# Performance work log

Measured on AMD Instinct MI355X. Metric: run time of the kernel, lower is better.

The kernel has to match this reference:

```python
import jax, jax.numpy as jnp
import numpy as np

N = 8192        # batch_size == num nodes == num hyperedges
D = 512         # hidden_dim
H_HEADS = 8
HD = D // H_HEADS
TOP_K = 16
EPS = 1e-5      # LayerNorm eps


def setup_inputs() -> dict:
    key = jax.random.key(0)
    ks = jax.random.split(key, 10)
    def rn(k, shape, scale=0.02):
        return jax.random.normal(k, shape, dtype=jnp.float32) * scale
    return {
        "x0": jax.random.normal(ks[0], (N, D), dtype=jnp.float32),
        "x1": jax.random.normal(ks[1], (N, D), dtype=jnp.float32),
        # modality projections: Linear -> ReLU -> LayerNorm (per modality)
        "w_p0": rn(ks[2], (D, D)), "b_p0": jnp.zeros((D,), jnp.float32),
        "g0": jnp.ones((D,), jnp.float32), "beta0": jnp.zeros((D,), jnp.float32),
        "w_p1": rn(ks[3], (D, D)), "b_p1": jnp.zeros((D,), jnp.float32),
        "g1": jnp.ones((D,), jnp.float32), "beta1": jnp.zeros((D,), jnp.float32),
        # MultiheadAttention packed in-proj + out-proj
        "in_w": rn(ks[4], (3 * D, D)), "in_b": jnp.zeros((3 * D,), jnp.float32),
        "out_w": rn(ks[5], (D, D)), "out_b": jnp.zeros((D,), jnp.float32),
        # edge weight predictor MLP
        "ew_w1": rn(ks[6], (D // 2, D)), "ew_b1": jnp.zeros((D // 2,), jnp.float32),
        "ew_w2": rn(ks[7], (1, D // 2)), "ew_b2": jnp.zeros((1,), jnp.float32),
    }


def _layernorm(x, g, b):
    m = x.mean(-1, keepdims=True)
    v = ((x - m) ** 2).mean(-1, keepdims=True)
    return (x - m) * jax.lax.rsqrt(v + EPS) * g + b


def _forward(x0, x1, w_p0, b_p0, g0, beta0, w_p1, b_p1, g1, beta1,
             in_w, in_b, out_w, out_b, ew_w1, ew_b1, ew_w2, ew_b2):
    # per-modality projection: Linear -> ReLU -> LayerNorm
    p0 = _layernorm(jax.nn.relu(x0 @ w_p0.T + b_p0), g0, beta0)
    p1 = _layernorm(jax.nn.relu(x1 @ w_p1.T + b_p1), g1, beta1)
    seq = jnp.stack([p0, p1], axis=1)                       # [N, 2, D]
    # cross-modal MHA (self-attention over the 2 modality tokens)
    qkv = seq @ in_w.T + in_b                               # [N, 2, 3D]
    q, k, v = jnp.split(qkv, 3, axis=-1)
    q = q.reshape(N, 2, H_HEADS, HD)
    k = k.reshape(N, 2, H_HEADS, HD)
    v = v.reshape(N, 2, H_HEADS, HD)
    scores = jnp.einsum('bqhd,bkhd->bhqk', q, k) / jnp.sqrt(jnp.float32(HD))
    attn = jax.nn.softmax(scores, axis=-1)                  # [N, h, 2, 2]
    ctx = jnp.einsum('bhqk,bkhd->bqhd', attn, v).reshape(N, 2, D)
    attended = ctx @ out_w.T + out_b                        # [N, 2, D]
    fused = attended.mean(axis=1)                           # [N, D]
    # node-node attention similarity, row-softmax
    sim = jax.nn.softmax(fused @ fused.T, axis=1)           # [N, N]
    _, idx = jax.lax.top_k(sim, TOP_K)                      # [N, K]
    vals = jnp.take_along_axis(sim, idx, axis=1)            # [N, K]
    rows = jnp.arange(N)
    # H[i,i]=1 first, then H[neighbor, i] = sim[i, neighbor] (may overwrite diag)
    H = jnp.zeros((N, N), sim.dtype).at[rows, rows].set(1.0)
    H = H.at[idx, rows[:, None]].set(vals)
    colsum = H.sum(axis=0)
    H = H.at[rows, rows].set(jnp.where(colsum == 0, 1.0, H[rows, rows]))
    # edge weights
    hidden = jax.nn.relu(fused @ ew_w1.T + ew_b1)
    ew = jax.nn.sigmoid(hidden @ ew_w2.T + ew_b2)[:, 0]     # [N]
    ew = jnp.maximum(ew, 1e-8)
    return H, ew


def reference(x0, x1, w_p0, b_p0, g0, beta0, w_p1, b_p1, g1, beta1,
              in_w, in_b, out_w, out_b, ew_w1, ew_b1, ew_w2, ew_b2):
    return _forward(x0, x1, w_p0, b_p0, g0, beta0, w_p1, b_p1, g1, beta1,
                    in_w, in_b, out_w, out_b, ew_w1, ew_b1, ew_w2, ew_b2)
```

## Files before the change

kernel.cpp:

```cpp
#include <hip/hip_runtime.h>
#include <hip/hip_bf16.h>

#define NN 8192
#define DD 512

typedef unsigned short u16;
typedef __bf16 bf16_t;
typedef bf16_t bf16x8 __attribute__((ext_vector_type(8)));
typedef float f32x4 __attribute__((ext_vector_type(4)));

__device__ __forceinline__ float bf2f(u16 h) {
    union { unsigned u; float f; } v; v.u = ((unsigned)h) << 16; return v.f;
}
__device__ __forceinline__ float bflo(unsigned u) {
    union { unsigned u; float f; } v; v.u = u << 16; return v.f;
}
__device__ __forceinline__ float bfhi(unsigned u) {
    union { unsigned u; float f; } v; v.u = u & 0xFFFF0000u; return v.f;
}
__device__ __forceinline__ u16 f2bf(float f) {
    union { float f; unsigned u; } v; v.f = f;
    unsigned r = v.u + 0x7fffu + ((v.u >> 16) & 1u);
    return (u16)(r >> 16);
}

__global__ __launch_bounds__(256) void cvt7(
        const float* __restrict__ s0, u16* __restrict__ d0,
        const float* __restrict__ s1, u16* __restrict__ d1,
        const float* __restrict__ s2, u16* __restrict__ d2,
        const float* __restrict__ s3, u16* __restrict__ d3,
        const float* __restrict__ s4, u16* __restrict__ d4,
        const float* __restrict__ s5, u16* __restrict__ d5,
        const float* __restrict__ s6, u16* __restrict__ d6) {
    size_t v = ((size_t)blockIdx.x * 256 + threadIdx.x) * 8;
    const float* s; u16* d; size_t off;
    if (v < 4194304)      { s = s0; d = d0; off = v; }
    else if (v < 8388608) { s = s1; d = d1; off = v - 4194304; }
    else if (v < 8650752) { s = s2; d = d2; off = v - 8388608; }
    else if (v < 8912896) { s = s3; d = d3; off = v - 8650752; }
    else if (v < 9699328) { s = s4; d = d4; off = v - 8912896; }
    else if (v < 9961472) { s = s5; d = d5; off = v - 9699328; }
    else                  { s = s6; d = d6; off = v - 9961472; }
    float4 a = *(const float4*)(s + off);
    float4 b = *(const float4*)(s + off + 4);
    ushort4 o0 = make_ushort4(f2bf(a.x), f2bf(a.y), f2bf(a.z), f2bf(a.w));
    ushort4 o1 = make_ushort4(f2bf(b.x), f2bf(b.y), f2bf(b.z), f2bf(b.w));
    *(ushort4*)(d + off) = o0;
    *(ushort4*)(d + off + 4) = o1;
}

#define EPS_LDS 136
template<bool RELU, bool BIAS, bool SPLIT>
__global__ __launch_bounds__(256) void gemm_bt(const u16* __restrict__ A,
        const u16* __restrict__ B, const float* __restrict__ bias,
        const u16* __restrict__ B2, const float* __restrict__ bias2, int halfY,
        u16* __restrict__ C, int M, int Nc, int K) {
    __shared__ alignas(16) u16 Smem[128 * 64 * 2];
    u16* As = Smem;
    u16* Bs = Smem + 128 * 64;
    const int t = threadIdx.x;
    const int lane = t & 63;
    const int wave = t >> 6;
    const int wm = (wave >> 1) * 64;
    const int wn = (wave & 1) * 64;
    const int rowA = blockIdx.y * 128;
    const int rowB = blockIdx.x * 128;
    if (SPLIT && (int)blockIdx.y >= halfY) { B = B2; bias = bias2; }

    f32x4 acc[4][4] = {};
    const int mrow = lane & 15;
    const int kk = (lane >> 4) * 8;

    for (int k0 = 0; k0 < K; k0 += 64) {
        __syncthreads();
        #pragma unroll
        for (int r = 0; r < 4; ++r) {
            int chunk = r * 256 + t;
            const u16* srcA = A + (size_t)(rowA + (chunk >> 3)) * K + k0 + (chunk & 7) * 8;
            __builtin_amdgcn_global_load_lds(
                (const __attribute__((address_space(1))) void*)srcA,
                (__attribute__((address_space(3))) void*)(As + chunk * 8), 16, 0, 0);
            const u16* srcB = B + (size_t)(rowB + (chunk >> 3)) * K + k0 + (chunk & 7) * 8;
            __builtin_amdgcn_global_load_lds(
                (const __attribute__((address_space(1))) void*)srcB,
                (__attribute__((address_space(3))) void*)(Bs + chunk * 8), 16, 0, 0);
        }
        __syncthreads();
        #pragma unroll
        for (int ks = 0; ks < 64; ks += 32) {
            bf16x8 af[4], bfv[4];
            #pragma unroll
            for (int i = 0; i < 4; ++i)
                af[i] = *(const bf16x8*)(As + (wm + i * 16 + mrow) * 64 + ks + kk);
            #pragma unroll
            for (int j = 0; j < 4; ++j)
                bfv[j] = *(const bf16x8*)(Bs + (wn + j * 16 + mrow) * 64 + ks + kk);
            #pragma unroll
            for (int i = 0; i < 4; ++i)
                #pragma unroll
                for (int j = 0; j < 4; ++j)
                    acc[i][j] = __builtin_amdgcn_mfma_f32_16x16x32_bf16(af[i], bfv[j], acc[i][j], 0, 0, 0);
        }
    }

    __syncthreads();
    const int lr0 = (lane >> 4) * 4;
    const int ec0 = wn + (lane & 15);
    #pragma unroll
    for (int h = 0; h < 2; ++h) {
        if ((wave >> 1) == h) {
            #pragma unroll
            for (int j = 0; j < 4; ++j) {
                int c = ec0 + j * 16;
                float bv = BIAS ? bias[rowB + c] : 0.0f;
                #pragma unroll
                for (int i = 0; i < 4; ++i) {
                    #pragma unroll
                    for (int r = 0; r < 4; ++r) {
                        float v = acc[i][j][r] + bv;
                        if (RELU) v = fmaxf(v, 0.0f);
                        Smem[(lr0 + i * 16 + r) * EPS_LDS + c] = f2bf(v);
                    }
                }
            }
        }
        __syncthreads();
        #pragma unroll
        for (int pass = 0; pass < 4; ++pass) {
            int chunk = pass * 256 + t;
            int rloc = chunk >> 4, coff = (chunk & 15) * 8;
            bf16x8 v = *(const bf16x8*)(Smem + rloc * EPS_LDS + coff);
            *(bf16x8*)(C + (size_t)(rowA + h * 64 + rloc) * Nc + rowB + coff) = v;
        }
        __syncthreads();
    }
}

__global__ __launch_bounds__(256) void gemm_qkv(const u16* __restrict__ A,
        const u16* __restrict__ B, const float* __restrict__ bias,
        u16* __restrict__ V, float* __restrict__ scores) {
    __shared__ alignas(16) u16 Smem[128 * 64 * 2];
    u16* As = Smem;
    u16* Bs = Smem + 128 * 64;
    const int t = threadIdx.x;
    const int lane = t & 63;
    const int wave = t >> 6;
    const int wm = (wave >> 1) * 64;
    const int wn = (wave & 1) * 64;
    const int c = blockIdx.x;
    const int rowA = blockIdx.y * 128;
    const bool isQK = (c < 8);

    f32x4 acc[4][4] = {};
    const int mrow = lane & 15;
    const int kk = (lane >> 4) * 8;

    for (int k0 = 0; k0 < DD; k0 += 64) {
        __syncthreads();
        #pragma unroll
        for (int r = 0; r < 4; ++r) {
            int chunk = r * 256 + t;
            int rr = chunk >> 3;
            int brow = isQK ? (c * 64 + rr + ((rr >= 64) ? 448 : 0))
                            : (1024 + (c - 8) * 128 + rr);
            const u16* srcA = A + (size_t)(rowA + rr) * DD + k0 + (chunk & 7) * 8;
            __builtin_amdgcn_global_load_lds(
                (const __attribute__((address_space(1))) void*)srcA,
                (__attribute__((address_space(3))) void*)(As + chunk * 8), 16, 0, 0);
            const u16* srcB = B + (size_t)brow * DD + k0 + (chunk & 7) * 8;
            __builtin_amdgcn_global_load_lds(
                (const __attribute__((address_space(1))) void*)srcB,
                (__attribute__((address_space(3))) void*)(Bs + chunk * 8), 16, 0, 0);
        }
        __syncthreads();
        #pragma unroll
        for (int ks = 0; ks < 64; ks += 32) {
            bf16x8 af[4], bfv[4];
            #pragma unroll
            for (int i = 0; i < 4; ++i)
                af[i] = *(const bf16x8*)(As + (wm + i * 16 + mrow) * 64 + ks + kk);
            #pragma unroll
            for (int j = 0; j < 4; ++j)
                bfv[j] = *(const bf16x8*)(Bs + (wn + j * 16 + mrow) * 64 + ks + kk);
            #pragma unroll
            for (int i = 0; i < 4; ++i)
                #pragma unroll
                for (int j = 0; j < 4; ++j)
                    acc[i][j] = __builtin_amdgcn_mfma_f32_16x16x32_bf16(af[i], bfv[j], acc[i][j], 0, 0, 0);
        }
    }

    __syncthreads();
    const int lr0 = (lane >> 4) * 4;
    const int ec0 = wn + (lane & 15);
    #pragma unroll
    for (int h = 0; h < 2; ++h) {
        if ((wave >> 1) == h) {
            #pragma unroll
            for (int j = 0; j < 4; ++j) {
                int cc = ec0 + j * 16;
                int bcol = isQK ? ((cc < 64) ? c * 64 + cc : 448 + c * 64 + cc)
                                : (1024 + (c - 8) * 128 + cc);
                float bv = bias[bcol];
                #pragma unroll
                for (int i = 0; i < 4; ++i) {
                    #pragma unroll
                    for (int r = 0; r < 4; ++r)
                        Smem[(lr0 + i * 16 + r) * EPS_LDS + cc] = f2bf(acc[i][j][r] + bv);
                }
            }
        }
        __syncthreads();
        if (isQK) {
            if (t < 128) {
                int nd = t >> 2, cb = t & 3, tt2 = cb >> 1, ss = cb & 1;
                const u16* qrow = Smem + (2 * nd + tt2) * EPS_LDS;
                const u16* krow = Smem + (2 * nd + ss) * EPS_LDS + 64;
                float s = 0.0f;
                #pragma unroll
                for (int d8 = 0; d8 < 8; ++d8) {
                    bf16x8 qv = *(const bf16x8*)(qrow + d8 * 8);
                    bf16x8 kv = *(const bf16x8*)(krow + d8 * 8);
                    #pragma unroll
                    for (int u = 0; u < 8; ++u) s += (float)qv[u] * (float)kv[u];
                }
                scores[(size_t)(rowA / 2 + h * 32 + nd) * 32 + c * 4 + cb] = s * 0.125f;
            }
        } else {
            #pragma unroll
            for (int pass = 0; pass < 4; ++pass) {
                int chunk = pass * 256 + t;
                int rloc = chunk >> 4, coff = (chunk & 15) * 8;
                bf16x8 v = *(const bf16x8*)(Smem + rloc * EPS_LDS + coff);
                *(bf16x8*)(V + (size_t)(rowA + h * 64 + rloc) * 512 + (c - 8) * 128 + coff) = v;
            }
        }
        __syncthreads();
    }
}

#define SYM_LDS 129
__global__ __launch_bounds__(256) void gemm_sym(const u16* __restrict__ F,
        u16* __restrict__ C) {
    __shared__ alignas(16) u16 Smem[128 * SYM_LDS];
    const int bx = blockIdx.x, by = blockIdx.y;
    if (bx < by) return;
    u16* As = Smem;
    u16* Bs = Smem + 128 * 64;
    const int t = threadIdx.x;
    const int lane = t & 63;
    const int wave = t >> 6;
    const int wm = (wave >> 1) * 64;
    const int wn = (wave & 1) * 64;
    const int rowI = by * 128;
    const int rowJ = bx * 128;

    f32x4 acc[4][4] = {};
    const int mrow = lane & 15;
    const int kk = (lane >> 4) * 8;

    for (int k0 = 0; k0 < DD; k0 += 64) {
        __syncthreads();
        #pragma unroll
        for (int r = 0; r < 4; ++r) {
            int chunk = r * 256 + t;
            const u16* srcA = F + (size_t)(rowI + (chunk >> 3)) * DD + k0 + (chunk & 7) * 8;
            __builtin_amdgcn_global_load_lds(
                (const __attribute__((address_space(1))) void*)srcA,
                (__attribute__((address_space(3))) void*)(As + chunk * 8), 16, 0, 0);
            const u16* srcB = F + (size_t)(rowJ + (chunk >> 3)) * DD + k0 + (chunk & 7) * 8;
            __builtin_amdgcn_global_load_lds(
                (const __attribute__((address_space(1))) void*)srcB,
                (__attribute__((address_space(3))) void*)(Bs + chunk * 8), 16, 0, 0);
        }
        __syncthreads();
        #pragma unroll
        for (int ks = 0; ks < 64; ks += 32) {
            bf16x8 af[4], bfv[4];
            #pragma unroll
            for (int i = 0; i < 4; ++i)
                af[i] = *(const bf16x8*)(As + (wm + i * 16 + mrow) * 64 + ks + kk);
            #pragma unroll
            for (int j = 0; j < 4; ++j)
                bfv[j] = *(const bf16x8*)(Bs + (wn + j * 16 + mrow) * 64 + ks + kk);
            #pragma unroll
            for (int i = 0; i < 4; ++i)
                #pragma unroll
                for (int j = 0; j < 4; ++j)
                    acc[i][j] = __builtin_amdgcn_mfma_f32_16x16x32_bf16(af[i], bfv[j], acc[i][j], 0, 0, 0);
        }
    }

    __syncthreads();
    const int er0 = wm + (lane >> 4) * 4;
    const int ec0 = wn + (lane & 15);
    #pragma unroll
    for (int j = 0; j < 4; ++j) {
        int c = ec0 + j * 16;
        #pragma unroll
        for (int i = 0; i < 4; ++i) {
            #pragma unroll
            for (int r = 0; r < 4; ++r)
                Smem[(er0 + i * 16 + r) * SYM_LDS + c] = f2bf(acc[i][j][r]);
        }
    }
    __syncthreads();
    #pragma unroll
    for (int pass = 0; pass < 8; ++pass) {
        int chunk = pass * 256 + t;
        int rloc = chunk >> 4, coff = (chunk & 15) * 8;
        union { u16 us[8]; bf16x8 v; } buf;
        #pragma unroll
        for (int k = 0; k < 8; ++k) buf.us[k] = Smem[rloc * SYM_LDS + coff + k];
        *(bf16x8*)(C + (size_t)(rowI + rloc) * NN + rowJ + coff) = buf.v;
    }
    if (bx != by) {
        #pragma unroll
        for (int pass = 0; pass < 8; ++pass) {
            int chunk = pass * 256 + t;
            int tr = chunk >> 4, roff = (chunk & 15) * 8;
            union { u16 us[8]; bf16x8 v; } buf;
            #pragma unroll
            for (int k = 0; k < 8; ++k) buf.us[k] = Smem[(roff + k) * SYM_LDS + tr];
            *(bf16x8*)(C + (size_t)(rowJ + tr) * NN + rowI + roff) = buf.v;
        }
    }
}

__global__ __launch_bounds__(256) void ln2_kernel(const u16* __restrict__ y,
        const float* __restrict__ g0, const float* __restrict__ b0,
        const float* __restrict__ g1, const float* __restrict__ b1,
        u16* __restrict__ seq) {
    int n = blockIdx.x * 4 + (threadIdx.x >> 6);
    int lane = threadIdx.x & 63;
    int modality = n >> 13, node = n & (NN - 1);
    const float* g = modality ? g1 : g0;
    const float* b = modality ? b1 : b0;
    bf16x8 v = *(const bf16x8*)(y + (size_t)n * DD + lane * 8);
    float x[8];
    float s = 0.0f;
    #pragma unroll
    for (int u = 0; u < 8; ++u) { x[u] = (float)v[u]; s += x[u]; }
    #pragma unroll
    for (int off = 32; off; off >>= 1) s += __shfl_xor(s, off);
    float mean = s * (1.0f / DD);
    float vs = 0.0f;
    #pragma unroll
    for (int u = 0; u < 8; ++u) { x[u] -= mean; vs += x[u] * x[u]; }
    #pragma unroll
    for (int off = 32; off; off >>= 1) vs += __shfl_xor(vs, off);
    float inv = rsqrtf(vs * (1.0f / DD) + 1e-5f);
    float4 ga = *(const float4*)(g + lane * 8);
    float4 gb = *(const float4*)(g + lane * 8 + 4);
    float4 ba = *(const float4*)(b + lane * 8);
    float4 bb = *(const float4*)(b + lane * 8 + 4);
    union { u16 us[8]; bf16x8 v; } o;
    o.us[0] = f2bf(x[0] * inv * ga.x + ba.x);
    o.us[1] = f2bf(x[1] * inv * ga.y + ba.y);
    o.us[2] = f2bf(x[2] * inv * ga.z + ba.z);
    o.us[3] = f2bf(x[3] * inv * ga.w + ba.w);
    o.us[4] = f2bf(x[4] * inv * gb.x + bb.x);
    o.us[5] = f2bf(x[5] * inv * gb.y + bb.y);
    o.us[6] = f2bf(x[6] * inv * gb.z + bb.z);
    o.us[7] = f2bf(x[7] * inv * gb.w + bb.w);
    *(bf16x8*)(seq + (size_t)node * (2 * DD) + modality * DD + lane * 8) = o.v;
}

__global__ __launch_bounds__(256) void attn_v(const float* __restrict__ scores,
        const u16* __restrict__ V, u16* __restrict__ ctxm) {
    int n = blockIdx.x * 4 + (threadIdx.x >> 6);
    int lane = threadIdx.x & 63;
    int h = lane >> 3;
    float4 sc = *(const float4*)(scores + (size_t)n * 32 + h * 4);
    float s00 = sc.x, s01 = sc.y, s10 = sc.z, s11 = sc.w;
    float m0 = fmaxf(s00, s01), e00 = __expf(s00 - m0), e01 = __expf(s01 - m0);
    float a00 = e00 / (e00 + e01), a01 = e01 / (e00 + e01);
    float m1 = fmaxf(s10, s11), e10 = __expf(s10 - m1), e11 = __expf(s11 - m1);
    float a10 = e10 / (e10 + e11), a11 = e11 / (e10 + e11);
    float al0 = 0.5f * (a00 + a10), al1 = 0.5f * (a01 + a11);
    bf16x8 v0 = *(const bf16x8*)(V + (size_t)(2 * n) * 512 + lane * 8);
    bf16x8 v1 = *(const bf16x8*)(V + (size_t)(2 * n + 1) * 512 + lane * 8);
    union { u16 us[8]; bf16x8 v; } o;
    #pragma unroll
    for (int u = 0; u < 8; ++u)
        o.us[u] = f2bf(al0 * (float)v0[u] + al1 * (float)v1[u]);
    *(bf16x8*)(ctxm + (size_t)n * 512 + lane * 8) = o.v;
}

__global__ __launch_bounds__(256) void topk_bf16(const u16* __restrict__ S,
        float* __restrict__ topv, int* __restrict__ topi) {
    const float NEG = -3e38f;
    int row = blockIdx.x * 4 + (threadIdx.x >> 6);
    int lane = threadIdx.x & 63;
    const u16* Sr = S + (size_t)row * NN;

    float m = NEG, l = 0.0f;
    float t1v = NEG, t2v = NEG;
    int t1i = 0x7FFFFFFF, t2i = 0x7FFFFFFF;

    #pragma unroll
    for (int p = 0; p < 16; ++p) {
        uint4 raw = *(const uint4*)(Sr + p * 512 + lane * 8);
        int base = p * 512 + lane * 8;
        #pragma unroll
        for (int q = 0; q < 4; ++q) {
            unsigned w = (&raw.x)[q];
            #pragma unroll
            for (int h = 0; h < 2; ++h) {
                float x = h ? bfhi(w) : bflo(w);
                int xi = base + q * 2 + h;
                if (x > m) { l = l * __expf(m - x) + 1.0f; m = x; }
                else l += __expf(x - m);
                bool g1 = x > t1v, g2 = x > t2v;
                t2v = g1 ? t1v : (g2 ? x : t2v);
                t2i = g1 ? t1i : (g2 ? xi : t2i);
                t1v = g1 ? x : t1v;
                t1i = g1 ? xi : t1i;
            }
        }
    }
    #pragma unroll
    for (int off = 32; off; off >>= 1) {
        float om = __shfl_xor(m, off);
        float ol = __shfl_xor(l, off);
        float nm = fmaxf(m, om);
        l = l * __expf(m - nm) + ol * __expf(om - nm);
        m = nm;
    }

    unsigned mk0 = 0, mk1 = 0, mk2 = 0, mk3 = 0;
    float cv = t1v; int ci = t1i;
    float bv = t2v; int bi = t2i;
    for (int r = 0; r < 16; ++r) {
        float wv = cv; int wi = ci;
        #pragma unroll
        for (int off = 32; off; off >>= 1) {
            float ov = __shfl_xor(wv, off);
            int oi = __shfl_xor(wi, off);
            if (ov > wv || (ov == wv && oi < wi)) { wv = ov; wi = oi; }
        }
        if (lane == 0) {
            topv[(size_t)row * 16 + r] = __expf(wv - m) / l;
            topi[(size_t)row * 16 + r] = wi;
        }
        if (wi == ci) {
            int slot = ((wi >> 9) << 3) | (wi & 7);
            unsigned bit = 1u << (slot & 31);
            if (slot < 32) mk0 |= bit; else if (slot < 64) mk1 |= bit;
            else if (slot < 96) mk2 |= bit; else mk3 |= bit;
            cv = bv; ci = bi;
            bv = NEG; bi = 0x7FFFFFFF;
            if (ci == 0x7FFFFFFF) {
                float nb = NEG; int ni = 0x7FFFFFFF;
                #pragma unroll
                for (int p = 0; p < 16; ++p) {
                    uint4 raw = *(const uint4*)(Sr + p * 512 + lane * 8);
                    int base = p * 512 + lane * 8;
                    #pragma unroll
                    for (int q = 0; q < 4; ++q) {
                        unsigned w = (&raw.x)[q];
                        #pragma unroll
                        for (int h = 0; h < 2; ++h) {
                            int sl = p * 8 + q * 2 + h;
                            unsigned mw = (sl < 32) ? mk0 : (sl < 64) ? mk1
                                        : (sl < 96) ? mk2 : mk3;
                            float x = ((mw >> (sl & 31)) & 1u) ? NEG
                                    : (h ? bfhi(w) : bflo(w));
                            if (x > nb) { nb = x; ni = base + q * 2 + h; }
                        }
                    }
                }
                cv = nb; ci = ni;
            }
        }
    }
}

__global__ __launch_bounds__(256) void scatter_diag(const float* __restrict__ topv,
        const int* __restrict__ topi, float* __restrict__ H) {
    int tk = blockIdx.x * 256 + threadIdx.x;
    if (tk < NN * 16) {
        int i = tk >> 4;
        int idx = topi[tk];
        H[(size_t)idx * NN + i] = topv[tk];
    } else {
        int c = tk - NN * 16;
        const int* ti = topi + c * 16;
        bool self = false;
        #pragma unroll
        for (int j = 0; j < 16; ++j) self |= (ti[j] == c);
        if (!self) H[(size_t)c * NN + c] = 1.0f;
    }
}

__global__ __launch_bounds__(256) void ew_kernel(const u16* __restrict__ hidden,
        const float* __restrict__ w2, const float* __restrict__ b2, float* __restrict__ out) {
    int n = blockIdx.x * 4 + (threadIdx.x >> 6);
    int lane = threadIdx.x & 63;
    const u16* hr = hidden + (size_t)n * 256;
    float s = 0.0f;
    #pragma unroll
    for (int p = 0; p < 4; ++p) s += bf2f(hr[lane + p * 64]) * w2[lane + p * 64];
    for (int off = 32; off; off >>= 1) s += __shfl_xor(s, off);
    if (lane == 0) {
        float z = s + b2[0];
        float sig = 1.0f / (1.0f + __expf(-z));
        out[n] = fmaxf(sig, 1e-8f);
    }
}

extern "C" void kernel_launch(void* const* d_in, const int* in_sizes, int n_in,
                              void* d_out, int out_size, void* d_ws, size_t ws_size,
                              hipStream_t stream) {
    const float* x0    = (const float*)d_in[0];
    const float* x1    = (const float*)d_in[1];
    const float* w_p0  = (const float*)d_in[2];
    const float* b_p0  = (const float*)d_in[3];
    const float* g0    = (const float*)d_in[4];
    const float* beta0 = (const float*)d_in[5];
    const float* w_p1  = (const float*)d_in[6];
    const float* b_p1  = (const float*)d_in[7];
    const float* g1    = (const float*)d_in[8];
    const float* beta1 = (const float*)d_in[9];
    const float* in_w  = (const float*)d_in[10];
    const float* in_b  = (const float*)d_in[11];
    const float* out_w = (const float*)d_in[12];
    const float* out_b = (const float*)d_in[13];
    const float* ew_w1 = (const float*)d_in[14];
    const float* ew_b1 = (const float*)d_in[15];
    const float* ew_w2 = (const float*)d_in[16];
    const float* ew_b2 = (const float*)d_in[17];

    float* Hf = (float*)d_out;
    float* ew_out = Hf + (size_t)NN * NN;

    u16* Hu = (u16*)d_out;
    u16* x0b    = Hu;
    u16* x1b    = Hu + 4194304;
    u16* y01    = Hu + 8388608;
    u16* seq    = Hu + 16777216;
    u16* Vbuf   = Hu + 25165824;
    u16* ctxm   = Hu + 50331648;
    u16* hidden = Hu + 54525952;
    float* scB  = (float*)(Hu + 58720256);
    u16* wp0b   = Hu + 60817408;
    u16* wp1b   = wp0b + 262144;
    u16* inwb   = wp1b + 262144;
    u16* outwb  = inwb + 786432;
    u16* eww1b  = outwb + 262144;
    u16* Sb     = Hu + 67108864;
    char* ws = (char*)d_ws;
    u16* fusedB = (u16*)ws;
    float* topv = (float*)(ws + (8u << 20));
    int*   topi = (int*)(ws + (8u << 20) + 524288);

    dim3 blk(256);
    const int BIG = 1 << 30;
    cvt7<<<dim3(4928), blk, 0, stream>>>(x0, x0b, x1, x1b, w_p0, wp0b, w_p1, wp1b,
                                         in_w, inwb, out_w, outwb, ew_w1, eww1b);
    gemm_bt<true, true, true><<<dim3(4, 128), blk, 0, stream>>>(
        x0b, wp0b, b_p0, wp1b, b_p1, 64, y01, 2 * NN, DD, DD);
    ln2_kernel<<<dim3(2 * NN / 4), blk, 0, stream>>>(y01, g0, beta0, g1, beta1, seq);
    gemm_qkv<<<dim3(12, 128), blk, 0, stream>>>(seq, inwb, in_b, Vbuf, scB);
    attn_v<<<dim3(NN / 4), blk, 0, stream>>>(scB, Vbuf, ctxm);
    gemm_bt<false, true, false><<<dim3(4, 64), blk, 0, stream>>>(
        ctxm, outwb, out_b, nullptr, nullptr, BIG, fusedB, NN, DD, DD);
    gemm_bt<true, true, false><<<dim3(2, 64), blk, 0, stream>>>(
        fusedB, eww1b, ew_b1, nullptr, nullptr, BIG, hidden, NN, 256, DD);
    ew_kernel<<<dim3(NN / 4), blk, 0, stream>>>(hidden, ew_w2, ew_b2, ew_out);
    gemm_sym<<<dim3(64, 64), blk, 0, stream>>>(fusedB, Sb);
    topk_bf16<<<dim3(NN / 4), blk, 0, stream>>>(Sb, topv, topi);
    hipMemsetAsync(Hf, 0, (size_t)NN * NN * sizeof(float), stream);
    scatter_diag<<<dim3((NN * 16 + NN) / 256), blk, 0, stream>>>(topv, topi, Hf);
}
```

Measured before the change: 692.6 us.

## Double-buffer gemm_bt K loop and fold edge-weight hidden GEMM into symmetric GEMM

gemm_bt now double-buffers its LDS tiles, so the global-to-LDS load of the next K slice is issued before the MFMA work on the current slice, and its epilogue writes the whole 128x128 tile in one pass instead of two halves. The edge-weight hidden GEMM (fused @ ew_w1^T with bias and ReLU) is folded into the symmetric similarity kernel as extra grid columns, which saves one launch and lets these small blocks run alongside the large sim GEMM. The cost is twice the LDS per block in gemm_bt, which may reduce occupancy, and a branchier combined kernel.

```diff
diff --git a/kernel.cpp b/kernel.cpp
--- a/kernel.cpp
+++ b/kernel.cpp
@@ -55,9 +55,7 @@
         const u16* __restrict__ B, const float* __restrict__ bias,
         const u16* __restrict__ B2, const float* __restrict__ bias2, int halfY,
         u16* __restrict__ C, int M, int Nc, int K) {
-    __shared__ alignas(16) u16 Smem[128 * 64 * 2];
-    u16* As = Smem;
-    u16* Bs = Smem + 128 * 64;
+    __shared__ alignas(16) u16 Smem[2][16384];
     const int t = threadIdx.x;
     const int lane = t & 63;
     const int wave = t >> 6;
@@ -70,9 +68,11 @@
     f32x4 acc[4][4] = {};
     const int mrow = lane & 15;
     const int kk = (lane >> 4) * 8;
-
-    for (int k0 = 0; k0 < K; k0 += 64) {
-        __syncthreads();
+    const int nt = K >> 6;
+
+    auto STAGE = [&](int buf, int k0) {
+        u16* As = Smem[buf];
+        u16* Bs = Smem[buf] + 8192;
         #pragma unroll
         for (int r = 0; r < 4; ++r) {
             int chunk = r * 256 + t;
@@ -85,7 +85,15 @@
                 (const __attribute__((address_space(1))) void*)srcB,
                 (__attribute__((address_space(3))) void*)(Bs + chunk * 8), 16, 0, 0);
         }
-        __syncthreads();
+    };
+
+    STAGE(0, 0);
+    __syncthreads();
+    int cur = 0;
+    for (int ti = 0; ti < nt; ++ti) {
+        if (ti + 1 < nt) STAGE(cur ^ 1, (ti + 1) << 6);
+        const u16* As = Smem[cur];
+        const u16* Bs = Smem[cur] + 8192;
         #pragma unroll
         for (int ks = 0; ks < 64; ks += 32) {
             bf16x8 af[4], bfv[4];
@@ -101,38 +109,34 @@
                 for (int j = 0; j < 4; ++j)
                     acc[i][j] = __builtin_amdgcn_mfma_f32_16x16x32_bf16(af[i], bfv[j], acc[i][j], 0, 0, 0);
         }
-    }
-
+        __syncthreads();
+        cur ^= 1;
+    }
+
+    u16* Ep = &Smem[0][0];
+    const int er0 = wm + (lane >> 4) * 4;
+    const int ec0 = wn + (lane & 15);
+    #pragma unroll
+    for (int j = 0; j < 4; ++j) {
+        int c = ec0 + j * 16;
+        float bv = BIAS ? bias[rowB + c] : 0.0f;
+        #pragma unroll
+        for (int i = 0; i < 4; ++i) {
+            #pragma unroll
+            for (int r = 0; r < 4; ++r) {
+                float v = acc[i][j][r] + bv;
+                if (RELU) v = fmaxf(v, 0.0f);
+                Ep[(er0 + i * 16 + r) * EPS_LDS + c] = f2bf(v);
+            }
+        }
+    }
     __syncthreads();
-    const int lr0 = (lane >> 4) * 4;
-    const int ec0 = wn + (lane & 15);
-    #pragma unroll
-    for (int h = 0; h < 2; ++h) {
-        if ((wave >> 1) == h) {
-            #pragma unroll
-            for (int j = 0; j < 4; ++j) {
-                int c = ec0 + j * 16;
-                float bv = BIAS ? bias[rowB + c] : 0.0f;
-                #pragma unroll
-                for (int i = 0; i < 4; ++i) {
-                    #pragma unroll
-                    for (int r = 0; r < 4; ++r) {
-                        float v = acc[i][j][r] + bv;
-                        if (RELU) v = fmaxf(v, 0.0f);
-                        Smem[(lr0 + i * 16 + r) * EPS_LDS + c] = f2bf(v);
-                    }
-                }
-            }
-        }
-        __syncthreads();
-        #pragma unroll
-        for (int pass = 0; pass < 4; ++pass) {
-            int chunk = pass * 256 + t;
-            int rloc = chunk >> 4, coff = (chunk & 15) * 8;
-            bf16x8 v = *(const bf16x8*)(Smem + rloc * EPS_LDS + coff);
-            *(bf16x8*)(C + (size_t)(rowA + h * 64 + rloc) * Nc + rowB + coff) = v;
-        }
-        __syncthreads();
+    #pragma unroll
+    for (int pass = 0; pass < 8; ++pass) {
+        int chunk = pass * 256 + t;
+        int rloc = chunk >> 4, coff = (chunk & 15) * 8;
+        bf16x8 v = *(const bf16x8*)(Ep + rloc * EPS_LDS + coff);
+        *(bf16x8*)(C + (size_t)(rowA + rloc) * Nc + rowB + coff) = v;
     }
 }
 
@@ -240,11 +244,13 @@
 }
 
 #define SYM_LDS 129
-__global__ __launch_bounds__(256) void gemm_sym(const u16* __restrict__ F,
-        u16* __restrict__ C) {
+__global__ __launch_bounds__(256) void gemm_symh(const u16* __restrict__ F,
+        u16* __restrict__ C, const u16* __restrict__ W1,
+        const float* __restrict__ b1, u16* __restrict__ Hid) {
     __shared__ alignas(16) u16 Smem[128 * SYM_LDS];
     const int bx = blockIdx.x, by = blockIdx.y;
-    if (bx < by) return;
+    const bool isHid = (bx >= 64);
+    if (!isHid && bx < by) return;
     u16* As = Smem;
     u16* Bs = Smem + 128 * 64;
     const int t = threadIdx.x;
@@ -253,7 +259,8 @@
     const int wm = (wave >> 1) * 64;
     const int wn = (wave & 1) * 64;
     const int rowI = by * 128;
-    const int rowJ = bx * 128;
+    const int rowJ = isHid ? (bx - 64) * 128 : bx * 128;
+    const u16* Bsrc = isHid ? W1 : F;
 
     f32x4 acc[4][4] = {};
     const int mrow = lane & 15;
@@ -268,7 +275,7 @@
             __builtin_amdgcn_global_load_lds(
                 (const __attribute__((address_space(1))) void*)srcA,
                 (__attribute__((address_space(3))) void*)(As + chunk * 8), 16, 0, 0);
-            const u16* srcB = F + (size_t)(rowJ + (chunk >> 3)) * DD + k0 + (chunk & 7) * 8;
+            const u16* srcB = Bsrc + (size_t)(rowJ + (chunk >> 3)) * DD + k0 + (chunk & 7) * 8;
             __builtin_amdgcn_global_load_lds(
                 (const __attribute__((address_space(1))) void*)srcB,
                 (__attribute__((address_space(3))) void*)(Bs + chunk * 8), 16, 0, 0);
@@ -297,14 +304,30 @@
     #pragma unroll
     for (int j = 0; j < 4; ++j) {
         int c = ec0 + j * 16;
+        float bv = isHid ? b1[rowJ + c] : 0.0f;
         #pragma unroll
         for (int i = 0; i < 4; ++i) {
             #pragma unroll
-            for (int r = 0; r < 4; ++r)
-                Smem[(er0 + i * 16 + r) * SYM_LDS + c] = f2bf(acc[i][j][r]);
+            for (int r = 0; r < 4; ++r) {
+                float v = acc[i][j][r] + bv;
+                if (isHid) v = fmaxf(v, 0.0f);
+                Smem[(er0 + i * 16 + r) * SYM_LDS + c] = f2bf(v);
+            }
         }
     }
     __syncthreads();
+    if (isHid) {
+        #pragma unroll
+        for (int pass = 0; pass < 8; ++pass) {
+            int chunk = pass * 256 + t;
+            int rloc = chunk >> 4, coff = (chunk & 15) * 8;
+            union { u16 us[8]; bf16x8 v; } buf;
+            #pragma unroll
+            for (int k = 0; k < 8; ++k) buf.us[k] = Smem[rloc * SYM_LDS + coff + k];
+            *(bf16x8*)(Hid + (size_t)(rowI + rloc) * 256 + rowJ + coff) = buf.v;
+        }
+        return;
+    }
     #pragma unroll
     for (int pass = 0; pass < 8; ++pass) {
         int chunk = pass * 256 + t;
@@ -565,10 +588,8 @@
     attn_v<<<dim3(NN / 4), blk, 0, stream>>>(scB, Vbuf, ctxm);
     gemm_bt<false, true, false><<<dim3(4, 64), blk, 0, stream>>>(
         ctxm, outwb, out_b, nullptr, nullptr, BIG, fusedB, NN, DD, DD);
-    gemm_bt<true, true, false><<<dim3(2, 64), blk, 0, stream>>>(
-        fusedB, eww1b, ew_b1, nullptr, nullptr, BIG, hidden, NN, 256, DD);
+    gemm_symh<<<dim3(66, 64), blk, 0, stream>>>(fusedB, Sb, eww1b, ew_b1, hidden);
     ew_kernel<<<dim3(NN / 4), blk, 0, stream>>>(hidden, ew_w2, ew_b2, ew_out);
-    gemm_sym<<<dim3(64, 64), blk, 0, stream>>>(fusedB, Sb);
     topk_bf16<<<dim3(NN / 4), blk, 0, stream>>>(Sb, topv, topi);
     hipMemsetAsync(Hf, 0, (size_t)NN * NN * sizeof(float), stream);
     scatter_diag<<<dim3((NN * 16 + NN) / 256), blk, 0, stream>>>(topv, topi, Hf);
```

New measurement: 656.4 us. 1.06x faster.
